# Kernel optimization log

Hardware: AMD Instinct MI355X
Metric: run time of the kernel (lower is better)

## Reference

```python
import jax, jax.numpy as jnp
import numpy as np

BIAS = 0.5       # triplet margin (self.bias)
EPS = 1e-8       # self.eps, threshold for counting positives
DIST_EPS = 1e-6  # eps inside sqrt for zero distances


def _euclidean_distance(x):
    # x: [N, D] -> pairwise Euclidean distance [N, N], matching torch impl exactly
    x2 = x @ x.T                      # [N, N] gram matrix
    sq = jnp.diag(x2)                 # [N] squared norms
    d = jax.nn.relu(sq[None, :] + sq[:, None] - 2.0 * x2)
    zero_mask = (d == 0.0).astype(x.dtype)
    # add eps where distance is exactly 0 to avoid sqrt(0) grad issues, then zero it back
    d = jnp.sqrt(d + zero_mask * DIST_EPS) * (1.0 - zero_mask)
    return d


def _valid_triplets(labels):
    # valid[i,j,k] = (i,j,k distinct) & (label[i]==label[j]) & (label[i]!=label[k])
    n = labels.shape[0]
    not_eye = ~jnp.eye(n, dtype=bool)
    distinct = not_eye[:, :, None] & not_eye[:, None, :] & not_eye[None, :, :]
    same = labels[None, :] == labels[:, None]          # same[i,j] = label[i]==label[j]
    valid = same[:, :, None] & ~same[:, None, :]
    return distinct & valid


def setup_inputs() -> dict:
    key = jax.random.key(0)
    k1, k2 = jax.random.split(key)
    embeddings = jax.random.normal(k1, (512, 128), dtype=jnp.float32)
    labels = jax.random.randint(k2, (512,), 0, 64, dtype=jnp.int64 if jax.config.jax_enable_x64 else jnp.int32)
    return {"embeddings": embeddings, "labels": labels}


def reference(embeddings, labels):
    d = _euclidean_distance(embeddings)                  # [N, N]
    # loss[i,j,k] = d(i,j) - d(i,k) + margin
    loss = d[:, :, None] - d[:, None, :] + BIAS          # [N, N, N]
    mask = _valid_triplets(labels).astype(loss.dtype)
    loss = jax.nn.relu(loss * mask)                      # mask applied BEFORE relu, as in torch
    num_positives = jnp.sum((loss > EPS).astype(loss.dtype))
    return jnp.sum(loss) / num_positives
```

## Files before the change

### kernel.cpp

```cpp
#include <hip/hip_runtime.h>

#define NPTS 512
#define DIM  128
#define MARGIN 0.5f
#define CNT_EPS 1e-8f
#define NBLK 256

__device__ __forceinline__ float dot4(float4 a, float4 b) {
    return a.x * b.x + a.y * b.y + a.z * b.z + a.w * b.w;
}

__global__ __launch_bounds__(1024, 4)
void triplet_row_kernel(const float* __restrict__ x,
                        const int* __restrict__ labels,
                        float* __restrict__ psum,
                        int* __restrict__ pcnt) {
    __shared__ float drow[2][NPTS];
    __shared__ float posv[2][NPTS];
    __shared__ int   lab[NPTS];
    __shared__ int   npos_sh[2];
    __shared__ float wsum[16];
    __shared__ int   wcnt[16];

    const int tid = threadIdx.x;
    const int h   = tid >> 9;
    const int t   = tid & 511;
    const int w8  = t >> 6;
    const int l   = tid & 63;
    const int g   = l >> 2;
    const int c   = l & 3;

    const int i  = 2 * blockIdx.x + h;

    if (tid < NPTS) lab[tid] = labels[tid];
    if (tid < 2)    npos_sh[tid] = 0;
    const int li = labels[i];

    const float4* xi4 = (const float4*)(x + i * DIM);
    float4 xf[8];
#pragma unroll
    for (int it = 0; it < 8; ++it) xf[it] = xi4[c + 4 * it];

    float sqi = 0.f;
#pragma unroll
    for (int it = 0; it < 8; ++it) sqi += dot4(xf[it], xf[it]);
    sqi += __shfl_xor(sqi, 1, 64);
    sqi += __shfl_xor(sqi, 2, 64);

#pragma unroll 2
    for (int pass = 0; pass < 4; ++pass) {
        const int j = pass * 128 + w8 * 16 + g;
        const float4* xj4 = (const float4*)(x + j * DIM);
        float dp = 0.f, sp = 0.f;
#pragma unroll
        for (int it = 0; it < 8; ++it) {
            float4 b = xj4[c + 4 * it];
            dp += dot4(b, xf[it]);
            sp += dot4(b, b);
        }
        dp += __shfl_xor(dp, 1, 64);
        dp += __shfl_xor(dp, 2, 64);
        sp += __shfl_xor(sp, 1, 64);
        sp += __shfl_xor(sp, 2, 64);
        if (c == 0) {
            float dsq = sqi + sp - 2.f * dp;
            dsq = dsq > 0.f ? dsq : 0.f;
            drow[h][j] = (dsq == 0.f) ? 0.f : sqrtf(dsq);
        }
    }
    __syncthreads();

    if (lab[t] == li && t != i) {
        int p = atomicAdd(&npos_sh[h], 1);
        posv[h][p] = drow[h][t] + MARGIN;
    }
    __syncthreads();
    const int npos = npos_sh[h];

    const bool  isneg = (lab[t] != li);
    const float dk    = drow[h][t];
    float lsum = 0.f;
    int   lcnt = 0;
    for (int p = 0; p < npos; ++p) {
        float v = posv[h][p] - dk;
        if (isneg && v > 0.f) {
            lsum += v;
            lcnt += (v > CNT_EPS) ? 1 : 0;
        }
    }

#pragma unroll
    for (int off = 1; off < 64; off <<= 1) {
        lsum += __shfl_xor(lsum, off, 64);
        lcnt += __shfl_xor(lcnt, off, 64);
    }
    const int wid = tid >> 6;
    if (l == 0) { wsum[wid] = lsum; wcnt[wid] = lcnt; }
    __syncthreads();
    if (tid == 0) {
        float s = 0.f;
        int   cc = 0;
#pragma unroll
        for (int q = 0; q < 16; ++q) { s += wsum[q]; cc += wcnt[q]; }
        psum[blockIdx.x] = s;
        pcnt[blockIdx.x] = cc;
    }
}

__global__ void finalize_kernel(const float4* __restrict__ psum4,
                                const int4* __restrict__ pcnt4,
                                float* __restrict__ out) {
    const int t = threadIdx.x;
    float4 a  = psum4[t];
    int4   ca = pcnt4[t];
    float s  = a.x + a.y + a.z + a.w;
    int   cc = ca.x + ca.y + ca.z + ca.w;
#pragma unroll
    for (int off = 1; off < 64; off <<= 1) {
        s  += __shfl_xor(s, off, 64);
        cc += __shfl_xor(cc, off, 64);
    }
    if (t == 0) out[0] = s / (float)cc;
}

extern "C" void kernel_launch(void* const* d_in, const int* in_sizes, int n_in,
                              void* d_out, int out_size, void* d_ws, size_t ws_size,
                              hipStream_t stream) {
    const float* x      = (const float*)d_in[0];
    const int*   labels = (const int*)d_in[1];
    float*       out    = (float*)d_out;

    float* psum = (float*)d_ws;
    int*   pcnt = (int*)(psum + NBLK);

    triplet_row_kernel<<<NBLK, 1024, 0, stream>>>(x, labels, psum, pcnt);
    finalize_kernel<<<1, 64, 0, stream>>>((const float4*)psum,
                                          (const int4*)pcnt, out);
}
```

Before: 16.60 us.

## Stage embedding chunks in swizzled shared memory with register prefetch

The two row-halves of a block (rows i and i+1) each read every x_j row directly from global memory. They now cooperatively stage 128-row chunks of x into XOR-swizzled LDS, prefetching the next chunk into registers while the current one is consumed. This halves the per-block global/L2 traffic for x and aims to avoid LDS bank conflicts. In exchange it adds 64KB of LDS per block, which limits occupancy, and extra __syncthreads barriers per chunk.

```diff
diff --git a/kernel.cpp b/kernel.cpp
--- a/kernel.cpp
+++ b/kernel.cpp
@@ -5,6 +5,9 @@
 #define MARGIN 0.5f
 #define CNT_EPS 1e-8f
 #define NBLK 256
+#define RPP 128
+#define F4R 32
+#define F4P (RPP * F4R)
 
 __device__ __forceinline__ float dot4(float4 a, float4 b) {
     return a.x * b.x + a.y * b.y + a.z * b.z + a.w * b.w;
@@ -15,6 +18,7 @@
                         const int* __restrict__ labels,
                         float* __restrict__ psum,
                         int* __restrict__ pcnt) {
+    __shared__ float4 buf[F4P];
     __shared__ float drow[2][NPTS];
     __shared__ float posv[2][NPTS];
     __shared__ int   lab[NPTS];
@@ -36,6 +40,8 @@
     if (tid < 2)    npos_sh[tid] = 0;
     const int li = labels[i];
 
+    const float4* x4 = (const float4*)x;
+
     const float4* xi4 = (const float4*)(x + i * DIM);
     float4 xf[8];
 #pragma unroll
@@ -47,14 +53,35 @@
     sqi += __shfl_xor(sqi, 1, 64);
     sqi += __shfl_xor(sqi, 2, 64);
 
-#pragma unroll 2
-    for (int pass = 0; pass < 4; ++pass) {
-        const int j = pass * 128 + w8 * 16 + g;
-        const float4* xj4 = (const float4*)(x + j * DIM);
+    {
+        float4 stg[4];
+#pragma unroll
+        for (int u = 0; u < 4; ++u) stg[u] = x4[tid + 1024 * u];
+#pragma unroll
+        for (int u = 0; u < 4; ++u) {
+            int v = tid + 1024 * u;
+            int r = v >> 5, m = v & 31;
+            buf[r * F4R + (m ^ (r & 7))] = stg[u];
+        }
+    }
+
+    for (int p = 0; p < 4; ++p) {
+        __syncthreads();
+
+        float4 nxt[4];
+        if (p < 3) {
+#pragma unroll
+            for (int u = 0; u < 4; ++u)
+                nxt[u] = x4[(p + 1) * F4P + tid + 1024 * u];
+        }
+
+        const int rl = w8 * 16 + g;
+        const int j  = p * RPP + rl;
+        const float4* brow = &buf[rl * F4R];
         float dp = 0.f, sp = 0.f;
 #pragma unroll
         for (int it = 0; it < 8; ++it) {
-            float4 b = xj4[c + 4 * it];
+            float4 b = brow[(c + 4 * it) ^ (rl & 7)];
             dp += dot4(b, xf[it]);
             sp += dot4(b, b);
         }
@@ -66,6 +93,16 @@
             float dsq = sqi + sp - 2.f * dp;
             dsq = dsq > 0.f ? dsq : 0.f;
             drow[h][j] = (dsq == 0.f) ? 0.f : sqrtf(dsq);
+        }
+
+        if (p < 3) {
+            __syncthreads();
+#pragma unroll
+            for (int u = 0; u < 4; ++u) {
+                int v = tid + 1024 * u;
+                int r = v >> 5, m = v & 31;
+                buf[r * F4R + (m ^ (r & 7))] = nxt[u];
+            }
         }
     }
     __syncthreads();
```

Result: slower. 28.82 us (+73.5%).

## Compute both anchor rows per thread to share x_j loads in half the threads

Applied to the files above, without the earlier changes.

Each block still handles two anchor rows, but now with 512 threads instead of 1024. Every thread computes both rows at once, so each x_j vector and its squared norm are loaded once and reused for two dot products. This halves global and L2 reads of the embedding matrix and removes the duplicated norm work. In exchange, per-thread register use doubles, each thread does twice the triplet-loop work, and there are fewer waves per block to hide latency.

```diff
diff --git a/kernel.cpp b/kernel.cpp
--- a/kernel.cpp
+++ b/kernel.cpp
@@ -10,7 +10,7 @@
     return a.x * b.x + a.y * b.y + a.z * b.z + a.w * b.w;
 }
 
-__global__ __launch_bounds__(1024, 4)
+__global__ __launch_bounds__(512, 2)
 void triplet_row_kernel(const float* __restrict__ x,
                         const int* __restrict__ labels,
                         float* __restrict__ psum,
@@ -19,73 +19,105 @@
     __shared__ float posv[2][NPTS];
     __shared__ int   lab[NPTS];
     __shared__ int   npos_sh[2];
-    __shared__ float wsum[16];
-    __shared__ int   wcnt[16];
+    __shared__ float wsum[8];
+    __shared__ int   wcnt[8];
 
     const int tid = threadIdx.x;
-    const int h   = tid >> 9;
-    const int t   = tid & 511;
-    const int w8  = t >> 6;
+    const int w   = tid >> 6;
     const int l   = tid & 63;
     const int g   = l >> 2;
     const int c   = l & 3;
 
-    const int i  = 2 * blockIdx.x + h;
+    const int i0 = 2 * blockIdx.x;
+    const int i1 = i0 + 1;
 
-    if (tid < NPTS) lab[tid] = labels[tid];
-    if (tid < 2)    npos_sh[tid] = 0;
-    const int li = labels[i];
+    lab[tid] = labels[tid];
+    if (tid < 2) npos_sh[tid] = 0;
+    const int li0 = labels[i0];
+    const int li1 = labels[i1];
 
-    const float4* xi4 = (const float4*)(x + i * DIM);
-    float4 xf[8];
+    const float4* xi0 = (const float4*)(x + i0 * DIM);
+    const float4* xi1 = (const float4*)(x + i1 * DIM);
+    float4 xf0[8], xf1[8];
 #pragma unroll
-    for (int it = 0; it < 8; ++it) xf[it] = xi4[c + 4 * it];
+    for (int it = 0; it < 8; ++it) xf0[it] = xi0[c + 4 * it];
+#pragma unroll
+    for (int it = 0; it < 8; ++it) xf1[it] = xi1[c + 4 * it];
 
-    float sqi = 0.f;
+    float sq0 = 0.f, sq1 = 0.f;
 #pragma unroll
-    for (int it = 0; it < 8; ++it) sqi += dot4(xf[it], xf[it]);
-    sqi += __shfl_xor(sqi, 1, 64);
-    sqi += __shfl_xor(sqi, 2, 64);
+    for (int it = 0; it < 8; ++it) {
+        sq0 += dot4(xf0[it], xf0[it]);
+        sq1 += dot4(xf1[it], xf1[it]);
+    }
+    sq0 += __shfl_xor(sq0, 1, 64);
+    sq0 += __shfl_xor(sq0, 2, 64);
+    sq1 += __shfl_xor(sq1, 1, 64);
+    sq1 += __shfl_xor(sq1, 2, 64);
 
 #pragma unroll 2
     for (int pass = 0; pass < 4; ++pass) {
-        const int j = pass * 128 + w8 * 16 + g;
+        const int j = pass * 128 + w * 16 + g;
         const float4* xj4 = (const float4*)(x + j * DIM);
-        float dp = 0.f, sp = 0.f;
+        float dp0 = 0.f, dp1 = 0.f, sp = 0.f;
 #pragma unroll
         for (int it = 0; it < 8; ++it) {
             float4 b = xj4[c + 4 * it];
-            dp += dot4(b, xf[it]);
-            sp += dot4(b, b);
+            dp0 += dot4(b, xf0[it]);
+            dp1 += dot4(b, xf1[it]);
+            sp  += dot4(b, b);
         }
-        dp += __shfl_xor(dp, 1, 64);
-        dp += __shfl_xor(dp, 2, 64);
-        sp += __shfl_xor(sp, 1, 64);
-        sp += __shfl_xor(sp, 2, 64);
+        dp0 += __shfl_xor(dp0, 1, 64);
+        dp0 += __shfl_xor(dp0, 2, 64);
+        dp1 += __shfl_xor(dp1, 1, 64);
+        dp1 += __shfl_xor(dp1, 2, 64);
+        sp  += __shfl_xor(sp, 1, 64);
+        sp  += __shfl_xor(sp, 2, 64);
         if (c == 0) {
-            float dsq = sqi + sp - 2.f * dp;
-            dsq = dsq > 0.f ? dsq : 0.f;
-            drow[h][j] = (dsq == 0.f) ? 0.f : sqrtf(dsq);
+            float dsq0 = sq0 + sp - 2.f * dp0;
+            float dsq1 = sq1 + sp - 2.f * dp1;
+            dsq0 = dsq0 > 0.f ? dsq0 : 0.f;
+            dsq1 = dsq1 > 0.f ? dsq1 : 0.f;
+            drow[0][j] = (dsq0 == 0.f) ? 0.f : sqrtf(dsq0);
+            drow[1][j] = (dsq1 == 0.f) ? 0.f : sqrtf(dsq1);
         }
     }
     __syncthreads();
 
-    if (lab[t] == li && t != i) {
-        int p = atomicAdd(&npos_sh[h], 1);
-        posv[h][p] = drow[h][t] + MARGIN;
+    if (lab[tid] == li0 && tid != i0) {
+        int p = atomicAdd(&npos_sh[0], 1);
+        posv[0][p] = drow[0][tid] + MARGIN;
+    }
+    if (lab[tid] == li1 && tid != i1) {
+        int p = atomicAdd(&npos_sh[1], 1);
+        posv[1][p] = drow[1][tid] + MARGIN;
     }
     __syncthreads();
-    const int npos = npos_sh[h];
+    const int npos0 = npos_sh[0];
+    const int npos1 = npos_sh[1];
 
-    const bool  isneg = (lab[t] != li);
-    const float dk    = drow[h][t];
     float lsum = 0.f;
     int   lcnt = 0;
-    for (int p = 0; p < npos; ++p) {
-        float v = posv[h][p] - dk;
-        if (isneg && v > 0.f) {
-            lsum += v;
-            lcnt += (v > CNT_EPS) ? 1 : 0;
+    {
+        const bool  isneg = (lab[tid] != li0);
+        const float dk    = drow[0][tid];
+        for (int p = 0; p < npos0; ++p) {
+            float v = posv[0][p] - dk;
+            if (isneg && v > 0.f) {
+                lsum += v;
+                lcnt += (v > CNT_EPS) ? 1 : 0;
+            }
+        }
+    }
+    {
+        const bool  isneg = (lab[tid] != li1);
+        const float dk    = drow[1][tid];
+        for (int p = 0; p < npos1; ++p) {
+            float v = posv[1][p] - dk;
+            if (isneg && v > 0.f) {
+                lsum += v;
+                lcnt += (v > CNT_EPS) ? 1 : 0;
+            }
         }
     }
 
@@ -94,14 +126,13 @@
         lsum += __shfl_xor(lsum, off, 64);
         lcnt += __shfl_xor(lcnt, off, 64);
     }
-    const int wid = tid >> 6;
-    if (l == 0) { wsum[wid] = lsum; wcnt[wid] = lcnt; }
+    if (l == 0) { wsum[w] = lsum; wcnt[w] = lcnt; }
     __syncthreads();
     if (tid == 0) {
         float s = 0.f;
         int   cc = 0;
 #pragma unroll
-        for (int q = 0; q < 16; ++q) { s += wsum[q]; cc += wcnt[q]; }
+        for (int q = 0; q < 8; ++q) { s += wsum[q]; cc += wcnt[q]; }
         psum[blockIdx.x] = s;
         pcnt[blockIdx.x] = cc;
     }
@@ -133,7 +164,7 @@
     float* psum = (float*)d_ws;
     int*   pcnt = (int*)(psum + NBLK);
 
-    triplet_row_kernel<<<NBLK, 1024, 0, stream>>>(x, labels, psum, pcnt);
+    triplet_row_kernel<<<NBLK, 512, 0, stream>>>(x, labels, psum, pcnt);
     finalize_kernel<<<1, 64, 0, stream>>>((const float4*)psum,
                                           (const int4*)pcnt, out);
 }
```

Result: faster. 15.08 us (-9.2%).
